# Kernel tuning notes

Measured on AMD Instinct MI355X. Metric: run time of the kernel, lower is better.

## Reference

```python
import math
import jax
import jax.numpy as jnp
import numpy as np
from jax import lax

B_, L, D_MODEL = 2, 1024, 2048
D_STATE, D_CONV, EXPAND = 16, 4, 2
D_INNER = EXPAND * D_MODEL          # 4096
DT_RANK = math.ceil(D_MODEL / 16)   # 128


def setup_inputs() -> dict:
    key = jax.random.key(0)
    ks = jax.random.split(key, 8)
    hidden_states = jax.random.normal(ks[0], (B_, L, D_MODEL), jnp.float32)
    in_proj_w = jax.random.normal(ks[1], (2 * D_INNER, D_MODEL), jnp.float32) * (D_MODEL ** -0.5)
    conv_w = jax.random.normal(ks[2], (D_INNER, D_CONV), jnp.float32) * (D_CONV ** -0.5)
    conv_b = jnp.zeros((D_INNER,), jnp.float32)
    x_proj_w = jax.random.normal(ks[3], (DT_RANK + 2 * D_STATE, D_INNER), jnp.float32) * (D_INNER ** -0.5)
    dt_std = DT_RANK ** -0.5
    dt_proj_w = jax.random.uniform(ks[4], (D_INNER, DT_RANK), jnp.float32, minval=-dt_std, maxval=dt_std)
    # dt bias init: softplus^{-1} of dt sampled log-uniform in [1e-3, 1e-1]
    dt = jnp.exp(jax.random.uniform(ks[5], (D_INNER,), jnp.float32)
                 * (math.log(0.1) - math.log(0.001)) + math.log(0.001))
    dt = jnp.clip(dt, 1e-4)
    dt_proj_b = dt + jnp.log(-jnp.expm1(-dt))
    A_log = jnp.log(jnp.broadcast_to(jnp.arange(1, D_STATE + 1, dtype=jnp.float32), (D_INNER, D_STATE)))
    D = jnp.ones((D_INNER,), jnp.float32)
    out_proj_w = jax.random.normal(ks[6], (D_MODEL, D_INNER), jnp.float32) * (D_INNER ** -0.5)
    return {
        'hidden_states': hidden_states, 'in_proj_w': in_proj_w,
        'conv_w': conv_w, 'conv_b': conv_b, 'x_proj_w': x_proj_w,
        'dt_proj_w': dt_proj_w, 'dt_proj_b': dt_proj_b,
        'A_log': A_log, 'D': D, 'out_proj_w': out_proj_w,
    }


def _silu(v):
    return v * jax.nn.sigmoid(v)


def _mamba_forward(hidden_states, in_proj_w, conv_w, conv_b, x_proj_w,
                   dt_proj_w, dt_proj_b, A_log, D, out_proj_w):
    b, l, _ = hidden_states.shape
    # in_proj: (b,l,d_model) -> (b, 2*d_inner, l)
    xz = jnp.einsum('bld,ed->bel', hidden_states, in_proj_w)
    x, z = xz[:, :D_INNER, :], xz[:, D_INNER:, :]
    A = -jnp.exp(A_log.astype(jnp.float32))  # (d_inner, d_state)
    # causal depthwise conv1d + SiLU
    xp = jnp.pad(x, ((0, 0), (0, 0), (D_CONV - 1, 0)))
    x = lax.conv_general_dilated(
        xp, conv_w[:, None, :], window_strides=(1,), padding='VALID',
        dimension_numbers=('NCH', 'OIH', 'NCH'), feature_group_count=D_INNER)
    x = _silu(x + conv_b[None, :, None])  # (b, d_inner, l)
    # x_proj -> dt, B, C
    x_dbl = jnp.einsum('bdl,kd->blk', x, x_proj_w)  # (b,l,dt_rank+2n)
    dt_lo = x_dbl[..., :DT_RANK]
    Bmat = x_dbl[..., DT_RANK:DT_RANK + D_STATE]          # (b,l,n)
    Cmat = x_dbl[..., DT_RANK + D_STATE:]                 # (b,l,n)
    delta = jax.nn.softplus(jnp.einsum('blr,dr->bld', dt_lo, dt_proj_w)
                            + dt_proj_b.astype(jnp.float32))  # (b,l,d)
    xt = jnp.transpose(x, (2, 0, 1))       # (l,b,d)
    dl = jnp.transpose(delta, (1, 0, 2))   # (l,b,d)
    Bl = jnp.transpose(Bmat, (1, 0, 2))    # (l,b,n)
    Cl = jnp.transpose(Cmat, (1, 0, 2))    # (l,b,n)

    def step(h, inp):
        d_t, B_t, C_t, x_t = inp
        dA = jnp.exp(d_t[..., None] * A)                       # (b,d,n)
        h = h * dA + d_t[..., None] * B_t[:, None, :] * x_t[..., None]
        y_t = jnp.sum(h * C_t[:, None, :], axis=-1)            # (b,d)
        return h, y_t

    h0 = jnp.zeros((b, D_INNER, D_STATE), jnp.float32)
    _, ys = lax.scan(step, h0, (dl, Bl, Cl, xt))  # ys: (l,b,d)
    y = jnp.transpose(ys, (1, 0, 2))              # (b,l,d)
    y = y + jnp.transpose(x, (0, 2, 1)) * D[None, None, :]
    y = y * _silu(jnp.transpose(z, (0, 2, 1)))
    out = jnp.einsum('bld,ed->ble', y, out_proj_w)  # (b,l,d_model)
    return out


def reference(hidden_states, in_proj_w, conv_w, conv_b, x_proj_w,
              dt_proj_w, dt_proj_b, A_log, D, out_proj_w):
    return _mamba_forward(hidden_states, in_proj_w, conv_w, conv_b, x_proj_w,
                          dt_proj_w, dt_proj_b, A_log, D, out_proj_w)
```

## Files before the change

### kernel.cpp

```cpp
#include <hip/hip_runtime.h>
#include <hip/hip_bf16.h>
#include <stdint.h>

#define BB 2
#define LL 1024
#define DMODEL 2048
#define DINNER 4096
#define DSTATE 16
#define DTRANK 128
#define XDBL_LD 256
#define CHUNK 64
#define NCH (LL / CHUNK)

typedef unsigned short ushort;
using short8 = __attribute__((ext_vector_type(8))) short;
using f32x16 = __attribute__((ext_vector_type(16))) float;
using us4    = __attribute__((ext_vector_type(4))) ushort;

__device__ __forceinline__ float bf2f(ushort u) {
    union { uint32_t i; float f; } v; v.i = ((uint32_t)u) << 16; return v.f;
}
__device__ __forceinline__ ushort f2bf(float f) {
    union { float f; uint32_t i; } v; v.f = f;
    uint32_t lsb = (v.i >> 16) & 1u;
    uint32_t r = v.i + 0x7FFFu + lsb;
    return (ushort)(r >> 16);
}

__device__ __forceinline__ void glds16(const ushort* g, ushort* l) {
    __builtin_amdgcn_global_load_lds(
        (const __attribute__((address_space(1))) void*)g,
        (__attribute__((address_space(3))) void*)l,
        16, 0, 0);
}

__global__ __launch_bounds__(256) void cvt_all(
    const float4* __restrict__ hidden, const float4* __restrict__ inproj,
    const float4* __restrict__ dtw, const float4* __restrict__ outp,
    const float4* __restrict__ xproj,
    us4* __restrict__ hid_h, us4* __restrict__ inp_h, us4* __restrict__ dtp_h,
    us4* __restrict__ outp_h, us4* __restrict__ xpp)
{
    long i = (long)blockIdx.x * 256 + threadIdx.x;
    const float4* src; us4* dst; long j;
    if (i < 1048576)      { src = hidden; dst = hid_h;  j = i; }
    else if (i < 5242880) { src = inproj; dst = inp_h;  j = i - 1048576; }
    else if (i < 5373952) { src = dtw;    dst = dtp_h;  j = i - 5242880; }
    else if (i < 7471104) { src = outp;   dst = outp_h; j = i - 5373952; }
    else {
        j = i - 7471104; dst = xpp;
        if (j >= 163840) { us4 z = {0, 0, 0, 0}; dst[j] = z; return; }
        src = xproj;
    }
    float4 v = src[j];
    us4 o; o.x = f2bf(v.x); o.y = f2bf(v.y); o.z = f2bf(v.z); o.w = f2bf(v.w);
    dst[j] = o;
}

template <int EPI, bool WF, bool WH>
__global__ __launch_bounds__(256) void gemm_nt(
    const ushort* __restrict__ A, int lda,
    const ushort* __restrict__ Bm, int ldb,
    float* __restrict__ Cf, ushort* __restrict__ Ch, int ldc,
    int K, const float* __restrict__ bias)
{
    __shared__ __align__(16) ushort sA[128 * 32];
    __shared__ __align__(16) ushort sB[128 * 32];

    const int tid  = threadIdx.x;
    const int lane = tid & 63;
    const int wave = tid >> 6;
    const int wr = wave >> 1, wc = wave & 1;

    const int NT = gridDim.x, MT = gridDim.y;
    int mt, nt;
    if ((NT & 7) == 0) {
        int lin   = blockIdx.y * NT + blockIdx.x;
        int strip = NT >> 3;
        int xcd   = lin & 7;
        int idx   = lin >> 3;
        nt = xcd * strip + (idx % strip);
        mt = idx / strip;
    } else { mt = blockIdx.y; nt = blockIdx.x; }
    const long m0 = (long)mt * 128;
    const long n0 = (long)nt * 128;

    const long zoff = (long)blockIdx.z;
    A  += zoff * (long)K;
    Bm += zoff * (long)K;
    const long Mrows = (long)MT * 128;
    if (WF) Cf += zoff * Mrows * (long)ldc;
    if (WH) Ch += zoff * Mrows * (long)ldc;

    f32x16 acc[2][2] = {};

    const int l31 = lane & 31;
    const int lhk = (lane >> 5) << 3;

    const int sr = tid >> 2;
    const int sc = (tid & 3) << 3;
    const ushort* Ag = A  + (m0 + sr) * (long)lda + sc;
    const ushort* Bg = Bm + (n0 + sr) * (long)ldb + sc;
    ushort* lA = sA + tid * 8;
    ushort* lB = sB + tid * 8;

    for (int k0 = 0; k0 < K; k0 += 32) {
        __syncthreads();
        glds16(Ag + k0, lA);
        glds16(Ag + 64 * (long)lda + k0, lA + 2048);
        glds16(Bg + k0, lB);
        glds16(Bg + 64 * (long)ldb + k0, lB + 2048);
        __syncthreads();

        short8 af[2][2], bfr[2][2];
        #pragma unroll
        for (int i = 0; i < 2; ++i)
            #pragma unroll
            for (int ks = 0; ks < 2; ++ks) {
                af[i][ks]  = *(const short8*)&sA[(wr * 64 + i * 32 + l31) * 32 + ks * 16 + lhk];
                bfr[i][ks] = *(const short8*)&sB[(wc * 64 + i * 32 + l31) * 32 + ks * 16 + lhk];
            }

        #pragma unroll
        for (int ks = 0; ks < 2; ++ks)
            #pragma unroll
            for (int i = 0; i < 2; ++i)
                #pragma unroll
                for (int j = 0; j < 2; ++j)
                    acc[i][j] = __builtin_amdgcn_mfma_f32_32x32x16_bf16(
                        af[i][ks], bfr[j][ks], acc[i][j], 0, 0, 0);
    }

    const int rq = (lane >> 5) << 2;
    #pragma unroll
    for (int i = 0; i < 2; ++i) {
        #pragma unroll
        for (int j = 0; j < 2; ++j) {
            long col = n0 + wc * 64 + j * 32 + l31;
            float bv = 0.f;
            if (EPI == 1) bv = bias[col];
            #pragma unroll
            for (int reg = 0; reg < 16; ++reg) {
                int rin = (reg & 3) + ((reg >> 2) << 3) + rq;
                long row = m0 + wr * 64 + i * 32 + rin;
                float v = acc[i][j][reg];
                if (EPI == 1) {
                    v += bv;
                    v = (v > 20.f) ? v : log1pf(__expf(v));
                }
                long idx = row * (long)ldc + col;
                if (WF) Cf[idx] = v;
                if (WH) Ch[idx] = f2bf(v);
            }
        }
    }
}

template <int NZ, bool WH_>
__global__ __launch_bounds__(256) void reduce_k(
    const float4* __restrict__ parts, long stride4, int n4,
    float4* __restrict__ outF, us4* __restrict__ outH)
{
    int i = blockIdx.x * 256 + threadIdx.x;
    if (i >= n4) return;
    float4 s = parts[i];
    #pragma unroll
    for (int z = 1; z < NZ; ++z) {
        float4 v = parts[(long)z * stride4 + i];
        s.x += v.x; s.y += v.y; s.z += v.z; s.w += v.w;
    }
    if (outF) outF[i] = s;
    if (WH_) {
        us4 o; o.x = f2bf(s.x); o.y = f2bf(s.y); o.z = f2bf(s.z); o.w = f2bf(s.w);
        outH[i] = o;
    }
}

__global__ __launch_bounds__(256) void conv_silu_kernel(
    const ushort* __restrict__ xz,
    const float* __restrict__ cw,
    const float* __restrict__ cb,
    ushort* __restrict__ xc)
{
    int gid = blockIdx.x * 256 + threadIdx.x;
    int d  = gid & (DINNER - 1);
    int rl = gid >> 12;
    int l  = rl & (LL - 1);
    float acc = cb[d];
    #pragma unroll
    for (int j = 0; j < 4; ++j) {
        int li = l - 3 + j;
        if (li >= 0)
            acc += cw[d * 4 + j] * bf2f(xz[(long)(rl - 3 + j) * 8192 + d]);
    }
    float s = acc / (1.f + __expf(-acc));
    xc[gid] = f2bf(s);
}

__global__ __launch_bounds__(256) void scan_p1(
    const ushort* __restrict__ delta,
    const ushort* __restrict__ xc,
    const float*  __restrict__ xdbl,
    const float*  __restrict__ A_log,
    float* __restrict__ Hbuf,
    float* __restrict__ sumdt_buf)
{
    __shared__ float sB[CHUNK * 16];
    const int tid = threadIdx.x;
    const int k = blockIdx.y, b = blockIdx.z;
    const int d = blockIdx.x * 256 + tid;
    const int row0 = b * LL + k * CHUNK;

    #pragma unroll
    for (int i = 0; i < 4; ++i) {
        int idx = i * 256 + tid;
        sB[idx] = xdbl[(long)(row0 + (idx >> 4)) * XDBL_LD + DTRANK + (idx & 15)];
    }
    __syncthreads();

    float A[DSTATE];
    const float4* Ap = (const float4*)(A_log + d * DSTATE);
    #pragma unroll
    for (int i = 0; i < 4; ++i) {
        float4 v = Ap[i];
        A[i*4+0] = -__expf(v.x); A[i*4+1] = -__expf(v.y);
        A[i*4+2] = -__expf(v.z); A[i*4+3] = -__expf(v.w);
    }

    float H[DSTATE];
    #pragma unroll
    for (int s = 0; s < DSTATE; ++s) H[s] = 0.f;
    float sumdt = 0.f;

    for (int t = 0; t < CHUNK; ++t) {
        const long row = row0 + t;
        const float dt = bf2f(delta[row * DINNER + d]);
        const float xv = bf2f(xc[row * DINNER + d]);
        const float dx = dt * xv;
        sumdt += dt;
        #pragma unroll
        for (int s = 0; s < DSTATE; ++s) {
            float dA = __expf(dt * A[s]);
            H[s] = H[s] * dA + dx * sB[t * 16 + s];
        }
    }

    const long o = ((long)(b * NCH + k) * DINNER + d) * DSTATE;
    float4* Ho = (float4*)(Hbuf + o);
    #pragma unroll
    for (int i = 0; i < 4; ++i) {
        float4 v; v.x = H[i*4+0]; v.y = H[i*4+1]; v.z = H[i*4+2]; v.w = H[i*4+3];
        Ho[i] = v;
    }
    sumdt_buf[(b * NCH + k) * DINNER + d] = sumdt;
}

__global__ __launch_bounds__(256) void scan_p2(
    const float* __restrict__ A_log,
    const float* __restrict__ sumdt_buf,
    float* __restrict__ Hbuf)
{
    int gid = blockIdx.x * 256 + threadIdx.x;
    int b = gid >> 16;
    int rem = gid & 65535;
    int d = rem >> 4, s = rem & 15;
    float A = -__expf(A_log[d * DSTATE + s]);
    float h = 0.f;
    for (int k = 0; k < NCH; ++k) {
        long idx = ((long)(b * NCH + k) * DINNER + d) * DSTATE + s;
        float Hk = Hbuf[idx];
        float sd = sumdt_buf[(b * NCH + k) * DINNER + d];
        Hbuf[idx] = h;
        h = h * __expf(A * sd) + Hk;
    }
}

__global__ __launch_bounds__(256) void scan_p3(
    const ushort* __restrict__ delta,
    const ushort* __restrict__ xc,
    const float*  __restrict__ xdbl,
    const ushort* __restrict__ xz,
    const float*  __restrict__ A_log,
    const float*  __restrict__ Dp,
    const float*  __restrict__ hin,
    ushort* __restrict__ y)
{
    __shared__ float sBC[CHUNK * 32];
    const int tid = threadIdx.x;
    const int k = blockIdx.y, b = blockIdx.z;
    const int d = blockIdx.x * 256 + tid;
    const int row0 = b * LL + k * CHUNK;

    #pragma unroll
    for (int i = 0; i < 8; ++i) {
        int idx = i * 256 + tid;
        sBC[idx] = xdbl[(long)(row0 + (idx >> 5)) * XDBL_LD + DTRANK + (idx & 31)];
    }
    __syncthreads();

    float A[DSTATE];
    const float4* Ap = (const float4*)(A_log + d * DSTATE);
    #pragma unroll
    for (int i = 0; i < 4; ++i) {
        float4 v = Ap[i];
        A[i*4+0] = -__expf(v.x); A[i*4+1] = -__expf(v.y);
        A[i*4+2] = -__expf(v.z); A[i*4+3] = -__expf(v.w);
    }
    const float Dd = Dp[d];

    float h[DSTATE];
    const float4* Hp = (const float4*)(hin + ((long)(b * NCH + k) * DINNER + d) * DSTATE);
    #pragma unroll
    for (int i = 0; i < 4; ++i) {
        float4 v = Hp[i];
        h[i*4+0] = v.x; h[i*4+1] = v.y; h[i*4+2] = v.z; h[i*4+3] = v.w;
    }

    for (int t = 0; t < CHUNK; ++t) {
        const long row = row0 + t;
        const float dt = bf2f(delta[row * DINNER + d]);
        const float xv = bf2f(xc[row * DINNER + d]);
        const float dx = dt * xv;
        float yt = 0.f;
        #pragma unroll
        for (int s = 0; s < DSTATE; ++s) {
            float dA = __expf(dt * A[s]);
            h[s] = h[s] * dA + dx * sBC[t * 32 + s];
            yt += h[s] * sBC[t * 32 + 16 + s];
        }
        yt += xv * Dd;
        const float zv = bf2f(xz[row * 8192 + DINNER + d]);
        yt *= zv / (1.f + __expf(-zv));
        y[row * DINNER + d] = f2bf(yt);
    }
}

extern "C" void kernel_launch(void* const* d_in, const int* in_sizes, int n_in,
                              void* d_out, int out_size, void* d_ws, size_t ws_size,
                              hipStream_t stream)
{
    const float* hidden    = (const float*)d_in[0];
    const float* in_proj   = (const float*)d_in[1];
    const float* conv_w    = (const float*)d_in[2];
    const float* conv_b    = (const float*)d_in[3];
    const float* x_proj    = (const float*)d_in[4];
    const float* dt_proj_w = (const float*)d_in[5];
    const float* dt_proj_b = (const float*)d_in[6];
    const float* A_log     = (const float*)d_in[7];
    const float* Dp        = (const float*)d_in[8];
    const float* out_proj  = (const float*)d_in[9];
    float* out = (float*)d_out;

    char* ws = (char*)d_ws;
    ushort* xz_h    = (ushort*)(ws);
    ushort* xc      = (ushort*)(ws + 33554432);
    ushort* xpp     = (ushort*)(ws + 50331648);
    float*  xdbl    = (float*)(ws + 52428800);
    ushort* xdblh   = (ushort*)(ws + 54525952);
    ushort* delta_h = (ushort*)(ws + 55574528);
    ushort* yb      = (ushort*)(ws + 72351744);
    ushort* hid_h   = (ushort*)(ws + 89128960);
    ushort* inp_h   = (ushort*)(ws + 97517568);
    float*  parts   = (float*)(ws + 97517568);
    float*  Hbuf    = (float*)(ws + 97517568);
    float*  sumdt   = (float*)(ws + 105906176);
    ushort* dtp_h   = (ushort*)(ws + 131072000);
    ushort* outp_h  = (ushort*)(ws + 132120576);

    const int M = BB * LL;

    cvt_all<<<30208, 256, 0, stream>>>(
        (const float4*)hidden, (const float4*)in_proj, (const float4*)dt_proj_w,
        (const float4*)out_proj, (const float4*)x_proj,
        (us4*)hid_h, (us4*)inp_h, (us4*)dtp_h, (us4*)outp_h, (us4*)xpp);

    gemm_nt<0, false, true><<<dim3(8192 / 128, M / 128), 256, 0, stream>>>(
        hid_h, DMODEL, inp_h, DMODEL, nullptr, xz_h, 8192, DMODEL, nullptr);

    conv_silu_kernel<<<(M * DINNER) / 256, 256, 0, stream>>>(xz_h, conv_w, conv_b, xc);

    gemm_nt<0, true, false><<<dim3(XDBL_LD / 128, M / 128, 16), 256, 0, stream>>>(
        xc, DINNER, xpp, DINNER, parts, nullptr, XDBL_LD, DINNER / 16, nullptr);
    reduce_k<16, true><<<(M * XDBL_LD / 4 + 255) / 256, 256, 0, stream>>>(
        (const float4*)parts, (long)M * XDBL_LD / 4, M * XDBL_LD / 4,
        (float4*)xdbl, (us4*)xdblh);

    gemm_nt<1, false, true><<<dim3(DINNER / 128, M / 128), 256, 0, stream>>>(
        xdblh, XDBL_LD, dtp_h, DTRANK, nullptr, delta_h, DINNER, DTRANK, dt_proj_b);

    scan_p1<<<dim3(DINNER / 256, NCH, BB), 256, 0, stream>>>(
        delta_h, xc, xdbl, A_log, Hbuf, sumdt);
    scan_p2<<<(BB * DINNER * DSTATE) / 256, 256, 0, stream>>>(
        A_log, sumdt, Hbuf);
    scan_p3<<<dim3(DINNER / 256, NCH, BB), 256, 0, stream>>>(
        delta_h, xc, xdbl, xz_h, A_log, Dp, Hbuf, yb);

    gemm_nt<0, true, false><<<dim3(DMODEL / 128, M / 128, 2), 256, 0, stream>>>(
        yb, DINNER, outp_h, DINNER, parts, nullptr, DMODEL, DINNER / 2, nullptr);
    reduce_k<2, false><<<(M * DMODEL / 4 + 255) / 256, 256, 0, stream>>>(
        (const float4*)parts, (long)M * DMODEL / 4, M * DMODEL / 4,
        (float4*)out, nullptr);
}
```

Before: 514.7 us.

## Switch GEMM to 16x16x32 MFMA with K-tile 64 and 4-way out_proj split-K

The shared GEMM kernel now stages a 64-wide K tile per iteration, which halves the number of barrier pairs per K. It replaces the 32x32x16 MFMA with 4x4 tiles of 16x16x32 MFMA and rewrites the LDS fragment indexing and the epilogue to match. The out_proj GEMM is split 4 ways over K instead of 2 to put more blocks on the device. Its partials go to a workspace region at offset 0 that reuses the no-longer-needed xz buffer, at the cost of more partial-sum traffic in the reduction. LDS use doubles per block, and the new unpadded row-major LDS layout may cause bank conflicts on the fragment reads.

```diff
diff --git a/kernel.cpp b/kernel.cpp
--- a/kernel.cpp
+++ b/kernel.cpp
@@ -14,7 +14,7 @@
 
 typedef unsigned short ushort;
 using short8 = __attribute__((ext_vector_type(8))) short;
-using f32x16 = __attribute__((ext_vector_type(16))) float;
+using f32x4  = __attribute__((ext_vector_type(4))) float;
 using us4    = __attribute__((ext_vector_type(4))) ushort;
 
 __device__ __forceinline__ float bf2f(ushort u) {
@@ -64,8 +64,8 @@
     float* __restrict__ Cf, ushort* __restrict__ Ch, int ldc,
     int K, const float* __restrict__ bias)
 {
-    __shared__ __align__(16) ushort sA[128 * 32];
-    __shared__ __align__(16) ushort sB[128 * 32];
+    __shared__ __align__(16) ushort sA[128 * 64];
+    __shared__ __align__(16) ushort sB[128 * 64];
 
     const int tid  = threadIdx.x;
     const int lane = tid & 63;
@@ -92,58 +92,59 @@
     if (WF) Cf += zoff * Mrows * (long)ldc;
     if (WH) Ch += zoff * Mrows * (long)ldc;
 
-    f32x16 acc[2][2] = {};
-
-    const int l31 = lane & 31;
-    const int lhk = (lane >> 5) << 3;
-
-    const int sr = tid >> 2;
-    const int sc = (tid & 3) << 3;
+    f32x4 acc[4][4] = {};
+
+    const int lrow = lane & 15;
+    const int lko  = (lane >> 4) << 3;
+
+    const int sr = tid >> 3;
+    const int sc = (tid & 7) << 3;
     const ushort* Ag = A  + (m0 + sr) * (long)lda + sc;
     const ushort* Bg = Bm + (n0 + sr) * (long)ldb + sc;
     ushort* lA = sA + tid * 8;
     ushort* lB = sB + tid * 8;
 
-    for (int k0 = 0; k0 < K; k0 += 32) {
+    for (int k0 = 0; k0 < K; k0 += 64) {
         __syncthreads();
-        glds16(Ag + k0, lA);
-        glds16(Ag + 64 * (long)lda + k0, lA + 2048);
-        glds16(Bg + k0, lB);
-        glds16(Bg + 64 * (long)ldb + k0, lB + 2048);
+        #pragma unroll
+        for (int c = 0; c < 4; ++c) {
+            glds16(Ag + (c * 32) * (long)lda + k0, lA + c * 2048);
+            glds16(Bg + (c * 32) * (long)ldb + k0, lB + c * 2048);
+        }
         __syncthreads();
 
-        short8 af[2][2], bfr[2][2];
         #pragma unroll
-        for (int i = 0; i < 2; ++i)
+        for (int ks = 0; ks < 2; ++ks) {
+            short8 af[4], bf[4];
             #pragma unroll
-            for (int ks = 0; ks < 2; ++ks) {
-                af[i][ks]  = *(const short8*)&sA[(wr * 64 + i * 32 + l31) * 32 + ks * 16 + lhk];
-                bfr[i][ks] = *(const short8*)&sB[(wc * 64 + i * 32 + l31) * 32 + ks * 16 + lhk];
-            }
-
+            for (int i = 0; i < 4; ++i)
+                af[i] = *(const short8*)&sA[(wr * 64 + i * 16 + lrow) * 64 + ks * 32 + lko];
+            #pragma unroll
+            for (int j = 0; j < 4; ++j)
+                bf[j] = *(const short8*)&sB[(wc * 64 + j * 16 + lrow) * 64 + ks * 32 + lko];
+
+            #pragma unroll
+            for (int i = 0; i < 4; ++i)
+                #pragma unroll
+                for (int j = 0; j < 4; ++j)
+                    acc[i][j] = __builtin_amdgcn_mfma_f32_16x16x32_bf16(
+                        af[i], bf[j], acc[i][j], 0, 0, 0);
+        }
+    }
+
+    const int r0 = (lane >> 4) * 4;
+    const int c0 = lane & 15;
+    #pragma unroll
+    for (int i = 0; i < 4; ++i) {
         #pragma unroll
-        for (int ks = 0; ks < 2; ++ks)
-            #pragma unroll
-            for (int i = 0; i < 2; ++i)
-                #pragma unroll
-                for (int j = 0; j < 2; ++j)
-                    acc[i][j] = __builtin_amdgcn_mfma_f32_32x32x16_bf16(
-                        af[i][ks], bfr[j][ks], acc[i][j], 0, 0, 0);
-    }
-
-    const int rq = (lane >> 5) << 2;
-    #pragma unroll
-    for (int i = 0; i < 2; ++i) {
-        #pragma unroll
-        for (int j = 0; j < 2; ++j) {
-            long col = n0 + wc * 64 + j * 32 + l31;
+        for (int j = 0; j < 4; ++j) {
+            long col = n0 + wc * 64 + j * 16 + c0;
             float bv = 0.f;
             if (EPI == 1) bv = bias[col];
             #pragma unroll
-            for (int reg = 0; reg < 16; ++reg) {
-                int rin = (reg & 3) + ((reg >> 2) << 3) + rq;
-                long row = m0 + wr * 64 + i * 32 + rin;
-                float v = acc[i][j][reg];
+            for (int r = 0; r < 4; ++r) {
+                long row = m0 + wr * 64 + i * 16 + r0 + r;
+                float v = acc[i][j][r];
                 if (EPI == 1) {
                     v += bv;
                     v = (v > 20.f) ? v : log1pf(__expf(v));
@@ -366,6 +367,7 @@
     float*  sumdt   = (float*)(ws + 105906176);
     ushort* dtp_h   = (ushort*)(ws + 131072000);
     ushort* outp_h  = (ushort*)(ws + 132120576);
+    float*  parts2  = (float*)(ws);
 
     const int M = BB * LL;
 
@@ -395,9 +397,9 @@
     scan_p3<<<dim3(DINNER / 256, NCH, BB), 256, 0, stream>>>(
         delta_h, xc, xdbl, xz_h, A_log, Dp, Hbuf, yb);
 
-    gemm_nt<0, true, false><<<dim3(DMODEL / 128, M / 128, 2), 256, 0, stream>>>(
-        yb, DINNER, outp_h, DINNER, parts, nullptr, DMODEL, DINNER / 2, nullptr);
-    reduce_k<2, false><<<(M * DMODEL / 4 + 255) / 256, 256, 0, stream>>>(
-        (const float4*)parts, (long)M * DMODEL / 4, M * DMODEL / 4,
+    gemm_nt<0, true, false><<<dim3(DMODEL / 128, M / 128, 4), 256, 0, stream>>>(
+        yb, DINNER, outp_h, DINNER, parts2, nullptr, DMODEL, DINNER / 4, nullptr);
+    reduce_k<4, false><<<(M * DMODEL / 4 + 255) / 256, 256, 0, stream>>>(
+        (const float4*)parts2, (long)M * DMODEL / 4, M * DMODEL / 4,
         (float4*)out, nullptr);
 }
```

Result: no change. 505.4 us (-1.8%).
